# Kernel tuning notes

Hardware: AMD Instinct MI355X
Metric: run time of the kernel (lower is better)

Reference implementation:

```python
import jax, jax.numpy as jnp
import numpy as np

E = 1024  # embed_dim

def setup_inputs() -> dict:
    key = jax.random.key(0)
    ks = jax.random.split(key, 7)
    s = 1.0 / np.sqrt(E)  # torch Linear default init scale (uniform bound)
    x = jax.random.normal(ks[0], (4, 2048, E), dtype=jnp.float32)
    Wq = jax.random.uniform(ks[1], (E, E), jnp.float32, -s, s)
    bq = jax.random.uniform(ks[2], (E,), jnp.float32, -s, s)
    Wk = jax.random.uniform(ks[3], (E, E), jnp.float32, -s, s)
    bk = jax.random.uniform(ks[4], (E,), jnp.float32, -s, s)
    Wv = jax.random.uniform(ks[5], (E, E), jnp.float32, -s, s)
    bv = jax.random.uniform(ks[6], (E,), jnp.float32, -s, s)
    return {"x": x, "Wq": Wq, "bq": bq, "Wk": Wk, "bk": bk, "Wv": Wv, "bv": bv}

def reference(x, Wq, bq, Wk, bk, Wv, bv):
    # torch nn.Linear: y = x @ W.T + b
    Q = jnp.einsum('bse,fe->bsf', x, Wq) + bq
    K = jnp.einsum('bse,fe->bsf', x, Wk) + bk
    V = jnp.einsum('bse,fe->bsf', x, Wv) + bv
    scale = jnp.sqrt(jnp.asarray(E, x.dtype))
    scores = jnp.einsum('bqd,bkd->bqk', Q, K) / scale  # [B,S,S]
    attn = jax.nn.softmax(scores, axis=-1)
    return jnp.einsum('bqk,bkd->bqd', attn, V)
```

## Files before the change

### kernel.cpp

```cpp
#include <hip/hip_runtime.h>
#include <hip/hip_bf16.h>


typedef __attribute__((ext_vector_type(8))) short bf16x8;
typedef __attribute__((ext_vector_type(4))) float f32x4;

#define DEVI static __device__ __forceinline__

DEVI short to_bf16(float f) {
    unsigned u = __builtin_bit_cast(unsigned, f);
    u += 0x7fffu + ((u >> 16) & 1u);
    return (short)(u >> 16);
}
DEVI float from_bf16(short s) {
    return __builtin_bit_cast(float, (unsigned)((unsigned short)s) << 16);
}

DEVI void gload_lds16(const short* g, short* l) {
    __builtin_amdgcn_global_load_lds(
        (const __attribute__((address_space(1))) void*)g,
        (__attribute__((address_space(3))) void*)l, 16, 0, 0);
}

template<int BM, int BN, int BIAS, typename TOUT>
__global__ __launch_bounds__(256, 2)
void gemm8(const short* __restrict__ A, long lda, long bsA,
           const short* __restrict__ B, long ldb, long bsB,
           const float* __restrict__ b0, const float* __restrict__ b1,
           const float* __restrict__ b2,
           TOUT* __restrict__ c0, TOUT* __restrict__ c1, TOUT* __restrict__ c2,
           long ldc, long bsC, int K, float scale)
{
    constexpr int MF = BM / 16;
    constexpr int NF = BN / 64;
    constexpr int RA = (BM * 32) / (8 * 256);
    constexpr int RB = (BN * 32) / (8 * 256);

    __shared__ __align__(16) short As[3 * BM * 32];
    __shared__ __align__(16) short Bs[3 * BN * 32];

    const int tid = threadIdx.x;
    const int z = blockIdx.z;
    const long m0 = (long)blockIdx.y * BM;
    const long n0 = (long)blockIdx.x * BN;
    const short* Ab = A + (long)z * bsA + m0 * lda;
    const short* Bb = B + (long)z * bsB + n0 * ldb;

    const int wn = tid >> 6;
    const int lane = tid & 63;
    const int lrow = lane & 15;
    const int q = lane >> 4;

    const int NT = K >> 5;

    auto stage = [&](int t, int b) {
        const long koff = (long)t * 32;
        #pragma unroll
        for (int i = 0; i < RA; ++i) {
            int s = i * 256 + tid;
            int row = s >> 2;
            int c = (s & 3) ^ ((row >> 1) & 3);
            gload_lds16(Ab + (long)row * lda + koff + c * 8,
                        &As[b * BM * 32 + s * 8]);
        }
        #pragma unroll
        for (int i = 0; i < RB; ++i) {
            int s = i * 256 + tid;
            int row = s >> 2;
            int c = (s & 3) ^ ((row >> 1) & 3);
            gload_lds16(Bb + (long)row * ldb + koff + c * 8,
                        &Bs[b * BN * 32 + s * 8]);
        }
    };

    f32x4 acc[MF][NF] = {};

    stage(0, 0);
    stage(1, 1);
    asm volatile("s_waitcnt vmcnt(6)" ::: "memory");
    __builtin_amdgcn_sched_barrier(0);
    __builtin_amdgcn_s_barrier();

    int b = 0;
    for (int t = 0; t < NT; ++t) {
        const short* Asb = &As[b * BM * 32];
        const short* Bsb = &Bs[b * BN * 32];

        bf16x8 bfr[NF];
        #pragma unroll
        for (int n = 0; n < NF; ++n) {
            int row = wn * 64 + n * 16 + lrow;
            int p = q ^ ((row >> 1) & 3);
            bfr[n] = *(const bf16x8*)&Bsb[row * 32 + p * 8];
        }
        bf16x8 af[MF];
        #pragma unroll
        for (int m = 0; m < MF; ++m) {
            int row = m * 16 + lrow;
            int p = q ^ ((row >> 1) & 3);
            af[m] = *(const bf16x8*)&Asb[row * 32 + p * 8];
        }

        if (t + 2 < NT) {
            int tb = b + 2; if (tb >= 3) tb -= 3;
            stage(t + 2, tb);
        }

        __builtin_amdgcn_s_setprio(1);
        #pragma unroll
        for (int m = 0; m < MF; ++m)
            #pragma unroll
            for (int n = 0; n < NF; ++n)
                acc[m][n] = __builtin_amdgcn_mfma_f32_16x16x32_bf16(
                    af[m], bfr[n], acc[m][n], 0, 0, 0);
        __builtin_amdgcn_s_setprio(0);

        if (t < NT - 1) {
            asm volatile("s_waitcnt lgkmcnt(0)" ::: "memory");
            asm volatile("s_waitcnt vmcnt(6)" ::: "memory");
            __builtin_amdgcn_sched_barrier(0);
            __builtin_amdgcn_s_barrier();
        }
        ++b; if (b == 3) b = 0;
    }

    const float* bias = (BIAS == 2) ? b0
                      : ((z == 0) ? b0 : (z == 1) ? b1 : b2);
    TOUT* Cz = ((z == 0) ? c0 : (z == 1) ? c1 : c2) + (long)z * bsC;
    TOUT* Cb = Cz + m0 * ldc + n0;
    #pragma unroll
    for (int m = 0; m < MF; ++m) {
        #pragma unroll
        for (int n = 0; n < NF; ++n) {
            #pragma unroll
            for (int r = 0; r < 4; ++r) {
                int row = m * 16 + q * 4 + r;
                int col = wn * 64 + n * 16 + lrow;
                float v = acc[m][n][r] * scale;
                if constexpr (BIAS == 1) v += bias[n0 + col];
                if constexpr (BIAS == 2) v += bias[m0 + row];
                if constexpr (sizeof(TOUT) == 2)
                    Cb[(long)row * ldc + col] = to_bf16(v);
                else
                    Cb[(long)row * ldc + col] = v;
            }
        }
    }
}

__global__ __launch_bounds__(256)
void cvt_f32_bf16(const float* __restrict__ src, short* __restrict__ dst, int n8)
{
    int i = blockIdx.x * 256 + threadIdx.x;
    if (i < n8) {
        float4 a = ((const float4*)src)[2 * i];
        float4 b = ((const float4*)src)[2 * i + 1];
        bf16x8 o = { to_bf16(a.x), to_bf16(a.y), to_bf16(a.z), to_bf16(a.w),
                     to_bf16(b.x), to_bf16(b.y), to_bf16(b.z), to_bf16(b.w) };
        *(bf16x8*)&dst[i * 8] = o;
    }
}

__global__ __launch_bounds__(256)
void cvt3_f32_bf16(const float* __restrict__ s0, const float* __restrict__ s1,
                   const float* __restrict__ s2, short* __restrict__ dst, int n8)
{
    int zz = blockIdx.y;
    const float* src = (zz == 0) ? s0 : (zz == 1) ? s1 : s2;
    int i = blockIdx.x * 256 + threadIdx.x;
    if (i < n8) {
        float4 a = ((const float4*)src)[2 * i];
        float4 b = ((const float4*)src)[2 * i + 1];
        bf16x8 o = { to_bf16(a.x), to_bf16(a.y), to_bf16(a.z), to_bf16(a.w),
                     to_bf16(b.x), to_bf16(b.y), to_bf16(b.z), to_bf16(b.w) };
        *(bf16x8*)&dst[(long)zz * n8 * 8 + i * 8] = o;
    }
}

__global__ __launch_bounds__(256)
void softmax_rows(short* __restrict__ S, int ncols)
{
    const long row = blockIdx.x;
    short* p = S + row * (long)ncols;
    const int t = threadIdx.x;

    union { bf16x8 v; short s[8]; } u;
    u.v = *(const bf16x8*)&p[t * 8];
    float f[8];
    float m = -3.0e38f;
    #pragma unroll
    for (int j = 0; j < 8; ++j) { f[j] = from_bf16(u.s[j]); m = fmaxf(m, f[j]); }
    #pragma unroll
    for (int off = 32; off > 0; off >>= 1) m = fmaxf(m, __shfl_xor(m, off));

    __shared__ float red[8];
    const int wave = t >> 6;
    if ((t & 63) == 0) red[wave] = m;
    __syncthreads();
    m = fmaxf(fmaxf(red[0], red[1]), fmaxf(red[2], red[3]));

    float sum = 0.f;
    #pragma unroll
    for (int j = 0; j < 8; ++j) { f[j] = __expf(f[j] - m); sum += f[j]; }
    #pragma unroll
    for (int off = 32; off > 0; off >>= 1) sum += __shfl_xor(sum, off);
    if ((t & 63) == 0) red[4 + wave] = sum;
    __syncthreads();
    sum = red[4] + red[5] + red[6] + red[7];

    const float inv = 1.0f / sum;
    #pragma unroll
    for (int j = 0; j < 8; ++j) u.s[j] = to_bf16(f[j] * inv);
    *(bf16x8*)&p[t * 8] = u.v;
}

extern "C" void kernel_launch(void* const* d_in, const int* in_sizes, int n_in,
                              void* d_out, int out_size, void* d_ws, size_t ws_size,
                              hipStream_t stream)
{
    (void)in_sizes; (void)n_in; (void)out_size; (void)ws_size;

    const float* x  = (const float*)d_in[0];
    const float* Wq = (const float*)d_in[1];
    const float* bq = (const float*)d_in[2];
    const float* Wk = (const float*)d_in[3];
    const float* bk = (const float*)d_in[4];
    const float* Wv = (const float*)d_in[5];
    const float* bv = (const float*)d_in[6];
    float* out = (float*)d_out;

    const int S = 2048, E = 1024;
    const long M1 = 1024l * 1024;

    short* w  = (short*)d_ws;
    short* Q  = w;
    short* Kb = w + 8 * M1;
    short* P  = w + 16 * M1;
    short* VT = w + 8 * M1;

    short* dows = (short*)d_out;
    short* xb = dows;
    short* Wb = dows + 8 * M1;

    dim3 blk(256);

    cvt_f32_bf16<<<dim3(4096), blk, 0, stream>>>(x, xb, (int)M1);
    cvt3_f32_bf16<<<dim3(512, 3), blk, 0, stream>>>(Wq, Wk, Wv, Wb, (int)(M1 / 8));

    gemm8<128, 256, 1, short><<<dim3(4, 64, 2), blk, 0, stream>>>(
        xb, E, 0, Wb, E, M1, bq, bk, nullptr, Q, Kb, nullptr, E, 0, E, 1.0f);

    gemm8<128, 256, 0, short><<<dim3(8, 16, 4), blk, 0, stream>>>(
        Q, E, 2 * M1, Kb, E, 2 * M1, nullptr, nullptr, nullptr,
        P, P, P, S, 4 * M1, E, 0.03125f);

    gemm8<128, 256, 2, short><<<dim3(8, 8, 4), blk, 0, stream>>>(
        Wb + 2 * M1, E, 0, xb, E, 2 * M1, bv, nullptr, nullptr,
        VT, VT, VT, S, 2 * M1, E, 1.0f);

    softmax_rows<<<dim3(4 * S), blk, 0, stream>>>(P, S);

    gemm8<128, 256, 0, float><<<dim3(4, 16, 4), blk, 0, stream>>>(
        P, S, 4 * M1, VT, S, 2 * M1, nullptr, nullptr, nullptr,
        out, out, out, E, 2 * M1, S, 1.0f);
}
```

Before: 187.0 us.

## Replace triple-buffered GEMM with single-buffer 128x128 K=64 tiles and swizzled block order

The GEMM kernel moves from 128x256 tiles with a three-stage K=32 LDS pipeline to 128x128 tiles with K=64 steps and a single LDS buffer. The 2x2 wave layout splits each wave's work across both M and N, and an XOR swizzle over 8 chunks per row replaces the old 4-chunk one. Block IDs are remapped in groups of 8 to improve L2 locality, and launch bounds ask for 3 blocks per CU. Dropping the prefetch pipeline means each K step now waits on its global loads before compute, trading less latency hiding for higher occupancy and fewer barriers per K.

```diff
diff --git a/kernel.cpp b/kernel.cpp
--- a/kernel.cpp
+++ b/kernel.cpp
@@ -22,106 +22,101 @@
         (__attribute__((address_space(3))) void*)l, 16, 0, 0);
 }
 
-template<int BM, int BN, int BIAS, typename TOUT>
-__global__ __launch_bounds__(256, 2)
-void gemm8(const short* __restrict__ A, long lda, long bsA,
-           const short* __restrict__ B, long ldb, long bsB,
-           const float* __restrict__ b0, const float* __restrict__ b1,
-           const float* __restrict__ b2,
-           TOUT* __restrict__ c0, TOUT* __restrict__ c1, TOUT* __restrict__ c2,
-           long ldc, long bsC, int K, float scale)
-{
-    constexpr int MF = BM / 16;
-    constexpr int NF = BN / 64;
-    constexpr int RA = (BM * 32) / (8 * 256);
-    constexpr int RB = (BN * 32) / (8 * 256);
-
-    __shared__ __align__(16) short As[3 * BM * 32];
-    __shared__ __align__(16) short Bs[3 * BN * 32];
+template<int BIAS, typename TOUT>
+__global__ __launch_bounds__(256, 3)
+void gemm97(const short* __restrict__ A, long lda, long bsA,
+            const short* __restrict__ B, long ldb, long bsB,
+            const float* __restrict__ b0, const float* __restrict__ b1,
+            const float* __restrict__ b2,
+            TOUT* __restrict__ c0, TOUT* __restrict__ c1, TOUT* __restrict__ c2,
+            long ldc, long bsC, int K, float scale)
+{
+    __shared__ __align__(16) short As[128 * 64];
+    __shared__ __align__(16) short Bs[128 * 64];
 
     const int tid = threadIdx.x;
     const int z = blockIdx.z;
-    const long m0 = (long)blockIdx.y * BM;
-    const long n0 = (long)blockIdx.x * BN;
+
+    const int gx = gridDim.x;
+    const int nwg = gx * gridDim.y;
+    const int id = blockIdx.y * gx + blockIdx.x;
+    const int id2 = (id & 7) * (nwg >> 3) + (id >> 3);
+    const long m0 = (long)(id2 / gx) * 128;
+    const long n0 = (long)(id2 % gx) * 128;
+
     const short* Ab = A + (long)z * bsA + m0 * lda;
     const short* Bb = B + (long)z * bsB + n0 * ldb;
 
-    const int wn = tid >> 6;
+    const int wv = tid >> 6;
     const int lane = tid & 63;
+    const int wr = (wv >> 1) * 64;
+    const int wc = (wv & 1) * 64;
     const int lrow = lane & 15;
     const int q = lane >> 4;
 
-    const int NT = K >> 5;
-
-    auto stage = [&](int t, int b) {
-        const long koff = (long)t * 32;
-        #pragma unroll
-        for (int i = 0; i < RA; ++i) {
+    const int NT = K >> 6;
+
+    auto stage = [&](int t) {
+        const long k0 = (long)t * 64;
+        #pragma unroll
+        for (int i = 0; i < 4; ++i) {
             int s = i * 256 + tid;
-            int row = s >> 2;
-            int c = (s & 3) ^ ((row >> 1) & 3);
-            gload_lds16(Ab + (long)row * lda + koff + c * 8,
-                        &As[b * BM * 32 + s * 8]);
-        }
-        #pragma unroll
-        for (int i = 0; i < RB; ++i) {
+            int row = s >> 3;
+            int src = (s & 7) ^ (row & 7);
+            gload_lds16(Ab + (long)row * lda + k0 + src * 8, &As[s * 8]);
+        }
+        #pragma unroll
+        for (int i = 0; i < 4; ++i) {
             int s = i * 256 + tid;
-            int row = s >> 2;
-            int c = (s & 3) ^ ((row >> 1) & 3);
-            gload_lds16(Bb + (long)row * ldb + koff + c * 8,
-                        &Bs[b * BN * 32 + s * 8]);
+            int row = s >> 3;
+            int src = (s & 7) ^ (row & 7);
+            gload_lds16(Bb + (long)row * ldb + k0 + src * 8, &Bs[s * 8]);
         }
     };
 
-    f32x4 acc[MF][NF] = {};
-
-    stage(0, 0);
-    stage(1, 1);
-    asm volatile("s_waitcnt vmcnt(6)" ::: "memory");
-    __builtin_amdgcn_sched_barrier(0);
-    __builtin_amdgcn_s_barrier();
-
-    int b = 0;
+    f32x4 acc[4][4] = {};
+
     for (int t = 0; t < NT; ++t) {
-        const short* Asb = &As[b * BM * 32];
-        const short* Bsb = &Bs[b * BN * 32];
-
-        bf16x8 bfr[NF];
-        #pragma unroll
-        for (int n = 0; n < NF; ++n) {
-            int row = wn * 64 + n * 16 + lrow;
-            int p = q ^ ((row >> 1) & 3);
-            bfr[n] = *(const bf16x8*)&Bsb[row * 32 + p * 8];
-        }
-        bf16x8 af[MF];
-        #pragma unroll
-        for (int m = 0; m < MF; ++m) {
-            int row = m * 16 + lrow;
-            int p = q ^ ((row >> 1) & 3);
-            af[m] = *(const bf16x8*)&Asb[row * 32 + p * 8];
-        }
-
-        if (t + 2 < NT) {
-            int tb = b + 2; if (tb >= 3) tb -= 3;
-            stage(t + 2, tb);
-        }
-
-        __builtin_amdgcn_s_setprio(1);
-        #pragma unroll
-        for (int m = 0; m < MF; ++m)
-            #pragma unroll
-            for (int n = 0; n < NF; ++n)
-                acc[m][n] = __builtin_amdgcn_mfma_f32_16x16x32_bf16(
-                    af[m], bfr[n], acc[m][n], 0, 0, 0);
-        __builtin_amdgcn_s_setprio(0);
-
-        if (t < NT - 1) {
+        if (t) {
             asm volatile("s_waitcnt lgkmcnt(0)" ::: "memory");
-            asm volatile("s_waitcnt vmcnt(6)" ::: "memory");
             __builtin_amdgcn_sched_barrier(0);
             __builtin_amdgcn_s_barrier();
         }
-        ++b; if (b == 3) b = 0;
+        stage(t);
+        asm volatile("s_waitcnt vmcnt(0)" ::: "memory");
+        __builtin_amdgcn_sched_barrier(0);
+        __builtin_amdgcn_s_barrier();
+
+        bf16x8 af[4][2], bf[4][2];
+        #pragma unroll
+        for (int m = 0; m < 4; ++m) {
+            int row = wr + m * 16 + lrow;
+            #pragma unroll
+            for (int kk = 0; kk < 2; ++kk) {
+                int ch = (kk * 4 + q) ^ (row & 7);
+                af[m][kk] = *(const bf16x8*)&As[row * 64 + ch * 8];
+            }
+        }
+        #pragma unroll
+        for (int n = 0; n < 4; ++n) {
+            int row = wc + n * 16 + lrow;
+            #pragma unroll
+            for (int kk = 0; kk < 2; ++kk) {
+                int ch = (kk * 4 + q) ^ (row & 7);
+                bf[n][kk] = *(const bf16x8*)&Bs[row * 64 + ch * 8];
+            }
+        }
+
+        __builtin_amdgcn_s_setprio(1);
+        #pragma unroll
+        for (int m = 0; m < 4; ++m)
+            #pragma unroll
+            for (int n = 0; n < 4; ++n)
+                #pragma unroll
+                for (int kk = 0; kk < 2; ++kk)
+                    acc[m][n] = __builtin_amdgcn_mfma_f32_16x16x32_bf16(
+                        af[m][kk], bf[n][kk], acc[m][n], 0, 0, 0);
+        __builtin_amdgcn_s_setprio(0);
     }
 
     const float* bias = (BIAS == 2) ? b0
@@ -129,13 +124,13 @@
     TOUT* Cz = ((z == 0) ? c0 : (z == 1) ? c1 : c2) + (long)z * bsC;
     TOUT* Cb = Cz + m0 * ldc + n0;
     #pragma unroll
-    for (int m = 0; m < MF; ++m) {
-        #pragma unroll
-        for (int n = 0; n < NF; ++n) {
+    for (int m = 0; m < 4; ++m) {
+        #pragma unroll
+        for (int n = 0; n < 4; ++n) {
             #pragma unroll
             for (int r = 0; r < 4; ++r) {
-                int row = m * 16 + q * 4 + r;
-                int col = wn * 64 + n * 16 + lrow;
+                int row = wr + m * 16 + q * 4 + r;
+                int col = wc + n * 16 + lrow;
                 float v = acc[m][n][r] * scale;
                 if constexpr (BIAS == 1) v += bias[n0 + col];
                 if constexpr (BIAS == 2) v += bias[m0 + row];
@@ -247,20 +242,20 @@
     cvt_f32_bf16<<<dim3(4096), blk, 0, stream>>>(x, xb, (int)M1);
     cvt3_f32_bf16<<<dim3(512, 3), blk, 0, stream>>>(Wq, Wk, Wv, Wb, (int)(M1 / 8));
 
-    gemm8<128, 256, 1, short><<<dim3(4, 64, 2), blk, 0, stream>>>(
+    gemm97<1, short><<<dim3(8, 64, 2), blk, 0, stream>>>(
         xb, E, 0, Wb, E, M1, bq, bk, nullptr, Q, Kb, nullptr, E, 0, E, 1.0f);
 
-    gemm8<128, 256, 0, short><<<dim3(8, 16, 4), blk, 0, stream>>>(
+    gemm97<0, short><<<dim3(16, 16, 4), blk, 0, stream>>>(
         Q, E, 2 * M1, Kb, E, 2 * M1, nullptr, nullptr, nullptr,
         P, P, P, S, 4 * M1, E, 0.03125f);
 
-    gemm8<128, 256, 2, short><<<dim3(8, 8, 4), blk, 0, stream>>>(
+    gemm97<2, short><<<dim3(16, 8, 4), blk, 0, stream>>>(
         Wb + 2 * M1, E, 0, xb, E, 2 * M1, bv, nullptr, nullptr,
         VT, VT, VT, S, 2 * M1, E, 1.0f);
 
     softmax_rows<<<dim3(4 * S), blk, 0, stream>>>(P, S);
 
-    gemm8<128, 256, 0, float><<<dim3(4, 16, 4), blk, 0, stream>>>(
+    gemm97<0, float><<<dim3(8, 16, 4), blk, 0, stream>>>(
         P, S, 4 * M1, VT, S, 2 * M1, nullptr, nullptr, nullptr,
         out, out, out, E, 2 * M1, S, 1.0f);
 }
```

After: 188.0 us. No clear change (+0.5%).
